# Kernel tuning notes

Measured on AMD Instinct MI355X. Metric: run time of the kernel, lower is better.

Reference implementation:

```python
import jax, jax.numpy as jnp
import numpy as np

SCORE_THR = 0.01
IOU_THR = 0.1          # NOTE: original layer hardcodes 0.1 in tf.image.non_max_suppression
MAX_DET = 100
NEG = jnp.float32(-1e30)


def _iou_one_vs_all(box, boxes):
    # box: [4] (y1,x1,y2,x2), boxes: [N,4]
    y1 = jnp.maximum(box[0], boxes[:, 0])
    x1 = jnp.maximum(box[1], boxes[:, 1])
    y2 = jnp.minimum(box[2], boxes[:, 2])
    x2 = jnp.minimum(box[3], boxes[:, 3])
    inter = jnp.maximum(y2 - y1, 0.0) * jnp.maximum(x2 - x1, 0.0)
    a = (box[2] - box[0]) * (box[3] - box[1])
    b = (boxes[:, 2] - boxes[:, 0]) * (boxes[:, 3] - boxes[:, 1])
    return inter / (a + b - inter + 1e-8)


def _nms_keep(boxes, scores):
    # Greedy NMS as a keep-mask over N anchors. Matches tf.image.non_max_suppression
    # restricted to anchors with score > SCORE_THR, up to MAX_DET selections.
    s = jnp.where(scores > SCORE_THR, scores, NEG)
    keep0 = jnp.zeros(s.shape, dtype=bool)

    def step(carry, _):
        s, keep = carry
        i = jnp.argmax(s)
        ok = s[i] > NEG * 0.5
        keep = keep.at[i].set(ok)
        iou = _iou_one_vs_all(boxes[i], boxes)
        s = jnp.where((iou > IOU_THR) & ok, NEG, s)
        s = s.at[i].set(NEG)
        return (s, keep), None

    (_, keep), _ = jax.lax.scan(step, (s, keep0), None, length=MAX_DET)
    return keep


def _filter_image(boxes_i, cls_i):
    # boxes_i: [N,4], cls_i: [N,C]
    C = cls_i.shape[1]
    # class-specific NMS: keep mask per class -> [C, N]
    keep = jax.vmap(lambda s: _nms_keep(boxes_i, s))(cls_i.T)
    keep_flat = keep.T.reshape(-1)          # [N*C], (anchor, class) flat order
    flat = cls_i.reshape(-1)                # [N*C]
    masked = jnp.where(keep_flat, flat, NEG)
    vals, idx = jax.lax.top_k(masked, MAX_DET)
    valid = vals > NEG * 0.5
    anchor = idx // C
    label = idx % C
    scores_out = jnp.where(valid, jnp.take(flat, idx), -1.0)
    boxes_out = jnp.where(valid[:, None], boxes_i[anchor], -1.0)
    labels_out = jnp.where(valid, label, -1).astype(jnp.int32)
    return boxes_out, scores_out, labels_out


def setup_inputs() -> dict:
    key = jax.random.key(0)
    k1, k2, k3 = jax.random.split(key, 3)
    B, N, C = 4, 49104, 90
    yx1 = jax.random.uniform(k1, (B, N, 2), dtype=jnp.float32) * 512.0
    hw = jax.random.uniform(k2, (B, N, 2), dtype=jnp.float32) * 128.0 + 1.0
    boxes = jnp.concatenate([yx1, yx1 + hw], axis=-1)          # [B,N,4] y1x1y2x2
    classification = jax.random.uniform(k3, (B, N, C), dtype=jnp.float32)
    return {"boxes": boxes, "classification": classification}


def reference(boxes, classification):
    return jax.vmap(_filter_image)(boxes, classification)
```

## Files before the change

### kernel.cpp

```cpp
#include <hip/hip_runtime.h>
#include <stdint.h>

typedef unsigned long long u64;

#define B_ 4
#define N_ 49104
#define C_ 90
#define NCLS (B_ * C_)
#define MAXK 100
#define THR 0.01f
#define NB2 2048
#define WIN 512
#define KCAP 4096
#define ACH 128
#define NCH ((N_ + ACH - 1) / ACH)
#define CAPC 32
#define NBIN_M 1280
#define BINBASE 0x3F6E0000u
#define BINSH_M 10

__device__ __forceinline__ float area_of(float y1, float x1, float y2, float x2) {
#pragma clang fp contract(off)
  return (y2 - y1) * (x2 - x1);
}

#define IOU_MID (26843547.0 / 268435456.0)

__device__ __forceinline__ bool iou_gt(float ay1, float ax1, float ay2, float ax2, float aa,
                                       float by1, float bx1, float by2, float bx2, float ba) {
#pragma clang fp contract(off)
  float y1 = fmaxf(ay1, by1);
  float x1 = fmaxf(ax1, bx1);
  float y2 = fminf(ay2, by2);
  float x2 = fminf(ax2, bx2);
  float inter = fmaxf(y2 - y1, 0.0f) * fmaxf(x2 - x1, 0.0f);
  float denom = aa + ba - inter + 1e-8f;
  return (double)inter >= IOU_MID * (double)denom;
}

__device__ __forceinline__ u64 umax64(u64 a, u64 b) { return a > b ? a : b; }

__device__ __forceinline__ u64 shfl_xor_u64(u64 v, int m) {
  int lo = __shfl_xor((int)(unsigned)v, m);
  int hi = __shfl_xor((int)(unsigned)(v >> 32), m);
  return ((u64)(unsigned)hi << 32) | (u64)(unsigned)lo;
}

__device__ __forceinline__ int key2bin_m(u64 k) {
  int d = (int)((unsigned)(k >> 32) - BINBASE);
  int bin = d >> BINSH_M;
  if (d < 0) bin = 0;
  if (bin > NBIN_M - 1) bin = NBIN_M - 1;
  return bin;
}

__global__ __launch_bounds__(256) void select_kernel(const float* __restrict__ cls,
                                                     u64* __restrict__ keybuf,
                                                     unsigned* __restrict__ cnt,
                                                     int capsel, float t0) {
  __shared__ u64 ll[C_ * CAPC];
  __shared__ unsigned lcnt[C_];
  __shared__ unsigned base_s[C_];
  int blk = blockIdx.x;
  int b = blk / NCH, ch = blk - b * NCH;
  int a0 = ch * ACH;
  int aEnd = a0 + ACH; if (aEnd > N_) aEnd = N_;
  int e0 = a0 * C_;
  int nelem = (aEnd - a0) * C_;
  int tid = threadIdx.x;

  for (int i = tid; i < C_; i += 256) lcnt[i] = 0u;
  __syncthreads();

  const float4* src4 = (const float4*)(cls + (size_t)b * N_ * C_ + e0);
  int n4 = nelem >> 2;
  for (int i4 = tid; i4 < n4; i4 += 256) {
    float4 v = src4[i4];
#pragma unroll
    for (int j = 0; j < 4; ++j) {
      float s = (&v.x)[j];
      if (s > t0) {
        int e = e0 + i4 * 4 + j;
        unsigned n = (unsigned)e / (unsigned)C_;
        unsigned c = (unsigned)e - n * (unsigned)C_;
        u64 key = ((u64)__float_as_uint(s) << 32) | (u64)(0xFFFFFFFFu - n);
        unsigned pos = atomicAdd(&lcnt[c], 1u);
        if (pos < CAPC) {
          ll[c * CAPC + pos] = key;
        } else {
          unsigned g = (unsigned)(b * C_) + c;
          unsigned gp = atomicAdd(&cnt[g * 16], 1u);
          if (gp < (unsigned)capsel) keybuf[(size_t)g * capsel + gp] = key;
        }
      }
    }
  }
  __syncthreads();

  if (tid < C_) {
    unsigned cc = lcnt[tid]; if (cc > CAPC) cc = CAPC;
    base_s[tid] = atomicAdd(&cnt[(b * C_ + tid) * 16], cc);
  }
  __syncthreads();

  for (int i = tid; i < C_ * CAPC; i += 256) {
    int c = i >> 5, j = i & 31;
    unsigned cc = lcnt[c]; if (cc > CAPC) cc = CAPC;
    if ((unsigned)j < cc) {
      unsigned pos = base_s[c] + (unsigned)j;
      if (pos < (unsigned)capsel)
        keybuf[(size_t)(b * C_ + c) * capsel + pos] = ll[i];
    }
  }
}

__global__ __launch_bounds__(512) void nms_kernel(const float* __restrict__ boxes,
                                                  const float* __restrict__ cls,
                                                  const u64* __restrict__ keybuf,
                                                  const unsigned* __restrict__ cnt,
                                                  unsigned* __restrict__ done,
                                                  int capsel, float t0,
                                                  u64* __restrict__ keepkeys,
                                                  int* __restrict__ nk_arr,
                                                  float* __restrict__ out) {
  int gcls = blockIdx.x;
  int b = gcls / C_, c = gcls - b * C_;
  __shared__ u64 karr[KCAP];
  __shared__ unsigned hist[NB2];
  __shared__ unsigned sfx[NB2];
  __shared__ float4 kb[MAXK];
  __shared__ float ka[MAXK];
  __shared__ unsigned wsum[8];
  __shared__ int sh_cnt[8];
  __shared__ int sh_last, sh_thr;
  __shared__ unsigned sh_cc;
  int tid = threadIdx.x;
  int lane = tid & 63;
  int wid = tid >> 6;

  for (int i = tid; i < MAXK; i += 512) keepkeys[(size_t)gcls * MAXK + i] = 0ull;
  for (int i = tid; i < NB2; i += 512) hist[i] = 0u;
  __syncthreads();

  unsigned Mraw = cnt[gcls * 16];
  bool overflow = (Mraw > (unsigned)capsel);
  int M = overflow ? 0 : (int)Mraw;

  const u64* src = keybuf + (size_t)gcls * capsel;

  const int PK = KCAP / 512;
  u64 kreg[PK];
#pragma unroll
  for (int q = 0; q < PK; ++q) {
    kreg[q] = 0ull;
    int i = q * 512 + tid;
    if (i < M) {
      kreg[q] = src[i];
      atomicAdd(&hist[(unsigned)(kreg[q] >> 44) & (NB2 - 1)], 1u);
    }
  }
  __syncthreads();

  {
    const int W = NB2 / 512;
    unsigned loc[W];
    unsigned psum = 0;
#pragma unroll
    for (int q = 0; q < W; ++q) {
      psum += hist[NB2 - 1 - (tid * W + q)];
      loc[q] = psum;
    }
    unsigned incl = psum;
#pragma unroll
    for (int s = 1; s < 64; s <<= 1) {
      unsigned v = (unsigned)__shfl_up((int)incl, s);
      if (lane >= s) incl += v;
    }
    if (lane == 63) wsum[wid] = incl;
    __syncthreads();
    unsigned bs = incl - psum;
    for (int w2 = 0; w2 < wid; ++w2) bs += wsum[w2];
#pragma unroll
    for (int q = 0; q < W; ++q)
      sfx[NB2 - 1 - (tid * W + q)] = bs + loc[q];
  }
  __syncthreads();

#pragma unroll
  for (int q = 0; q < PK; ++q) {
    int i = q * 512 + tid;
    if (i < M) {
      u64 k = kreg[q];
      unsigned bin = (unsigned)(k >> 44) & (NB2 - 1);
      unsigned old = atomicSub(&hist[bin], 1u);
      karr[sfx[bin] - old] = k;
    }
  }
  __syncthreads();

  {
    u64 mk2[PK]; int mt[PK];
#pragma unroll
    for (int q = 0; q < PK; ++q) {
      mk2[q] = 0ull; mt[q] = -1;
      int i = q * 512 + tid;
      if (i < M) {
        u64 k = karr[i];
        int bin = (int)((unsigned)(k >> 44) & (NB2 - 1));
        int hi2 = (int)sfx[bin];
        int lo2 = (bin == NB2 - 1) ? 0 : (int)sfx[bin + 1];
        int r = lo2;
        for (int j = lo2; j < hi2; ++j) r += (karr[j] > k);
        mk2[q] = k; mt[q] = r;
      }
    }
    __syncthreads();
#pragma unroll
    for (int q = 0; q < PK; ++q)
      if (mt[q] >= 0) karr[mt[q]] = mk2[q];
  }
  __syncthreads();

  const float4* bx4 = (const float4*)(boxes + (size_t)b * N_ * 4);

  int seen = 0;
  int nwin = (M + WIN - 1) / WIN;
  for (int w = 0; w < nwin && seen < MAXK; ++w) {
    int base = w * WIN;
    int ci = base + tid;
    bool have = ci < M;
    float4 cb = make_float4(0.f, 0.f, 0.f, 0.f);
    float ca = 0.f;
    if (have) {
      u64 k = karr[ci];
      cb = bx4[0xFFFFFFFFu - (unsigned)(k & 0xFFFFFFFFull)];
      ca = area_of(cb.x, cb.y, cb.z, cb.w);
    }
    bool dead = !have;
    for (int j = 0; j < seen; ++j) {
      float4 sb = kb[j]; float sa = ka[j];
      dead |= iou_gt(sb.x, sb.y, sb.z, sb.w, sa,
                     cb.x, cb.y, cb.z, cb.w, ca);
    }
    u64 alive = __ballot(!dead);

    int nslice = (((M - base) < WIN ? (M - base) : WIN) + 63) >> 6;
    for (int s = 0; s < nslice; ++s) {
      if (wid == s) {
        int nkl = seen;
        int slo = base + (s << 6);
        while (alive != 0ull && nkl < MAXK) {
          int bit = __ffsll((long long)alive) - 1;
          float sy1 = __shfl(cb.x, bit);
          float sx1 = __shfl(cb.y, bit);
          float sy2 = __shfl(cb.z, bit);
          float sx2 = __shfl(cb.w, bit);
          float sa  = __shfl(ca,   bit);
          if (lane == 0) {
            u64 key = karr[slo + bit];
            unsigned anchor = 0xFFFFFFFFu - (unsigned)(key & 0xFFFFFFFFull);
            unsigned flat = anchor * C_ + (unsigned)c;
            keepkeys[(size_t)gcls * MAXK + nkl] =
                (key & 0xFFFFFFFF00000000ull) | (u64)(0xFFFFFFFFu - flat);
            kb[nkl] = make_float4(sy1, sx1, sy2, sx2);
            ka[nkl] = sa;
          }
          ++nkl;
          alive &= ~__ballot(iou_gt(sy1, sx1, sy2, sx2, sa,
                                    cb.x, cb.y, cb.z, cb.w, ca));
        }
        if (lane == 0) sh_cnt[s] = nkl;
        seen = nkl;
      }
      __syncthreads();
      int nkNew = (wid == s) ? seen : sh_cnt[s];
      if (nkNew >= MAXK) { seen = nkNew; break; }
      if (wid > s && nkNew > seen) {
        bool d2 = false;
        for (int j = seen; j < nkNew; ++j) {
          float4 sb = kb[j]; float sa = ka[j];
          d2 |= iou_gt(sb.x, sb.y, sb.z, sb.w, sa,
                       cb.x, cb.y, cb.z, cb.w, ca);
        }
        alive &= __ballot(!d2);
      }
      seen = nkNew;
    }
  }

  int nkF = seen;
  if (nkF < MAXK) {
    float teff = overflow ? 2.0f : t0;
    const float* sbase = cls + (size_t)b * N_ * C_ + c;
    const float* bx = boxes + (size_t)b * N_ * 4;
    u64* kkp = keepkeys + (size_t)gcls * MAXK;
    u64* red = karr;
    int nk2 = nkF;
    while (nk2 < MAXK) {
      u64 best = 0ull;
      for (int n = tid; n < N_; n += 512) {
        float s = sbase[(size_t)n * C_];
        if (s > THR && s <= teff) {
          float y1 = bx[(size_t)n * 4 + 0], x1 = bx[(size_t)n * 4 + 1];
          float y2 = bx[(size_t)n * 4 + 2], x2 = bx[(size_t)n * 4 + 3];
          float ar = area_of(y1, x1, y2, x2);
          bool ov = false;
          for (int j = 0; j < nk2; ++j) {
            float4 kbj = kb[j];
            if (iou_gt(kbj.x, kbj.y, kbj.z, kbj.w, ka[j], y1, x1, y2, x2, ar)) { ov = true; break; }
          }
          if (!ov) {
            u64 key = ((u64)__float_as_uint(s) << 32) | (u64)(0xFFFFFFFFu - (unsigned)n);
            best = umax64(best, key);
          }
        }
      }
      red[tid] = best;
      __syncthreads();
      for (int sft = 256; sft > 0; sft >>= 1) {
        if (tid < sft) red[tid] = umax64(red[tid], red[tid + sft]);
        __syncthreads();
      }
      u64 sel = red[0];
      __syncthreads();
      if (sel == 0ull) {
        if (tid == 0) {
          unsigned target2 = 0xFFFFFFFFu - (unsigned)c;
          for (int j = 0; j < nk2; ++j)
            if ((unsigned)(kkp[j] & 0xFFFFFFFFull) == target2) kkp[j] = 0ull;
        }
        break;
      }
      unsigned anchor = 0xFFFFFFFFu - (unsigned)(sel & 0xFFFFFFFFull);
      if (tid == 0) {
        float y1 = bx[(size_t)anchor * 4 + 0], x1 = bx[(size_t)anchor * 4 + 1];
        float y2 = bx[(size_t)anchor * 4 + 2], x2 = bx[(size_t)anchor * 4 + 3];
        kb[nk2] = make_float4(y1, x1, y2, x2);
        ka[nk2] = area_of(y1, x1, y2, x2);
        unsigned flat = anchor * C_ + (unsigned)c;
        kkp[nk2] = (sel & 0xFFFFFFFF00000000ull) | (u64)(0xFFFFFFFFu - flat);
      }
      ++nk2;
      __syncthreads();
    }
    nkF = nk2;
  }
  if (tid == 0) nk_arr[gcls] = nkF;

  __syncthreads();
  if (tid == 0) {
    __threadfence();
    sh_last = (atomicAdd(&done[b], 1u) == (unsigned)(C_ - 1)) ? 1 : 0;
  }
  __syncthreads();
  if (!sh_last) return;
  __threadfence();

  {
    const u64* kk = keepkeys + (size_t)b * C_ * MAXK;
    const int TOT = C_ * MAXK;
    unsigned* histm = hist;
    unsigned* sfxm = sfx;
    u64* mk = karr;
    u64* selk = karr + 512;

    for (int i = tid; i < NBIN_M; i += 512) histm[i] = 0u;
    if (tid == 0) { sh_thr = -1; sh_cc = 0u; }
    __syncthreads();
    for (int i = tid; i < TOT; i += 512) {
      u64 k = kk[i];
      if (k != 0ull) atomicAdd(&histm[key2bin_m(k)], 1u);
    }
    __syncthreads();

    const int Wm = 3;
    int j0 = tid * Wm;
    unsigned psum = 0;
#pragma unroll
    for (int q = 0; q < Wm; ++q) {
      int bin = NBIN_M - 1 - (j0 + q);
      if (bin >= 0) psum += histm[bin];
    }
    unsigned incl = psum;
#pragma unroll
    for (int s = 1; s < 64; s <<= 1) {
      unsigned v = (unsigned)__shfl_up((int)incl, s);
      if (lane >= s) incl += v;
    }
    if (lane == 63) wsum[wid] = incl;
    __syncthreads();
    unsigned base = incl - psum;
    for (int w2 = 0; w2 < wid; ++w2) base += wsum[w2];
    unsigned running = base;
    int mythr = -1;
#pragma unroll
    for (int q = 0; q < Wm; ++q) {
      int bin = NBIN_M - 1 - (j0 + q);
      if (bin >= 0) {
        running += histm[bin];
        sfxm[bin] = running;
        if (mythr < 0 && running >= (unsigned)MAXK) mythr = bin;
      }
    }
    if (mythr >= 0) atomicMax(&sh_thr, mythr);
    __syncthreads();

    int thr = sh_thr; if (thr < 0) thr = 0;
    unsigned S = sfxm[thr];

    if (S <= 512u) {
      for (int i = tid; i < TOT; i += 512) {
        u64 k = kk[i];
        if (k != 0ull && key2bin_m(k) >= thr) {
          unsigned pos = atomicAdd(&sh_cc, 1u);
          mk[pos] = k;
        }
      }
      __syncthreads();
      for (int i = (int)S + tid; i < 512; i += 512) mk[i] = 0ull;
      __syncthreads();
      for (int k2 = 2; k2 <= 512; k2 <<= 1) {
        for (int j = k2 >> 1; j > 0; j >>= 1) {
          if (tid < 256) {
            int i1 = 2 * tid - (tid & (j - 1));
            int i2 = i1 | j;
            u64 a = mk[i1], bb2 = mk[i2];
            bool desc = ((i1 & k2) == 0);
            bool sw = desc ? (a < bb2) : (a > bb2);
            if (sw) { mk[i1] = bb2; mk[i2] = a; }
          }
          __syncthreads();
        }
      }
      for (int r = tid; r < MAXK; r += 512) selk[r] = mk[r];
      __syncthreads();
    } else {
      if (wid == 0) {
        int c0 = lane, c1 = lane + 64;
        int len0 = (c0 < C_) ? nk_arr[b * C_ + c0] : 0;
        int len1 = (c1 < C_) ? nk_arr[b * C_ + c1] : 0;
        int h0 = 0, h1 = 0;
        auto fetchc = [&](int cc, int& h, int len) -> u64 {
          while (h < len) {
            u64 k = kk[(size_t)cc * MAXK + h];
            if (k != 0ull) return k;
            ++h;
          }
          return 0ull;
        };
        u64 cand0 = (c0 < C_) ? fetchc(c0, h0, len0) : 0ull;
        u64 cand1 = (c1 < C_) ? fetchc(c1, h1, len1) : 0ull;
        for (int r = 0; r < MAXK; ++r) {
          u64 my = umax64(cand0, cand1);
          u64 g = my;
#pragma unroll
          for (int m = 1; m < 64; m <<= 1) g = umax64(g, shfl_xor_u64(g, m));
          if (lane == 0) selk[r] = g;
          if (g != 0ull && my == g) {
            if (cand0 == g) { ++h0; cand0 = fetchc(c0, h0, len0); }
            else            { ++h1; cand1 = fetchc(c1, h1, len1); }
          }
        }
      }
      __syncthreads();
    }

    for (int r = tid; r < MAXK; r += 512) {
      u64 s = selk[r];
      float oy1, ox1, oy2, ox2, sc, lb;
      if (s != 0ull) {
        unsigned flat = 0xFFFFFFFFu - (unsigned)(s & 0xFFFFFFFFull);
        unsigned anchor = flat / C_;
        unsigned label = flat - anchor * C_;
        sc = __uint_as_float((unsigned)(s >> 32));
        const float4 bp = ((const float4*)(boxes + (size_t)b * N_ * 4))[anchor];
        oy1 = bp.x; ox1 = bp.y; oy2 = bp.z; ox2 = bp.w;
        lb = (float)label;
      } else {
        oy1 = ox1 = oy2 = ox2 = -1.0f; sc = -1.0f; lb = -1.0f;
      }
      float* bo = out + ((size_t)b * MAXK + r) * 4;
      bo[0] = oy1; bo[1] = ox1; bo[2] = oy2; bo[3] = ox2;
      out[(size_t)B_ * MAXK * 4 + b * MAXK + r] = sc;
      out[(size_t)B_ * MAXK * 4 + B_ * MAXK + b * MAXK + r] = lb;
    }
  }
}

extern "C" void kernel_launch(void* const* d_in, const int* in_sizes, int n_in,
                              void* d_out, int out_size, void* d_ws, size_t ws_size,
                              hipStream_t stream) {
  const float* boxes = (const float*)d_in[0];
  const float* cls = (const float*)d_in[1];
  char* ws = (char*)d_ws;

  int capsel; float t0;
  auto need_for = [](int cap) -> size_t {
    return 23104 + (size_t)NCLS * cap * 8 + 288000 + 1440;
  };
  if (ws_size >= need_for(4096))      { capsel = 4096; t0 = 0.93f;  }
  else if (ws_size >= need_for(2048)) { capsel = 2048; t0 = 0.962f; }
  else                                { capsel = 1024; t0 = 0.985f; }

  unsigned* cnt = (unsigned*)ws;
  unsigned* done = (unsigned*)(ws + 23040);
  u64* keybuf = (u64*)(ws + 23104);
  size_t off = 23104 + (size_t)NCLS * capsel * 8;
  u64* keepkeys = (u64*)(ws + off);      off += 288000;
  int* nk_arr = (int*)(ws + off);

  hipMemsetAsync(ws, 0, 23104, stream);
  select_kernel<<<B_ * NCH, 256, 0, stream>>>(cls, keybuf, cnt, capsel, t0);
  nms_kernel<<<NCLS, 512, 0, stream>>>(boxes, cls, keybuf, cnt, done, capsel, t0,
                                       keepkeys, nk_arr, (float*)d_out);
}
```

Baseline: 185.5 us.

## Sort and NMS only a top-score prefix per class, fall back to rescan

```diff
diff --git a/kernel.cpp b/kernel.cpp
--- a/kernel.cpp
+++ b/kernel.cpp
@@ -10,8 +10,9 @@
 #define MAXK 100
 #define THR 0.01f
 #define NB2 2048
-#define WIN 512
-#define KCAP 4096
+#define KCAP 640
+#define PTGT 448
+#define PCAP 512
 #define ACH 128
 #define NCH ((N_ + ACH - 1) / ACH)
 #define CAPC 32
@@ -132,6 +133,7 @@
   __shared__ float ka[MAXK];
   __shared__ unsigned wsum[8];
   __shared__ int sh_cnt[8];
+  __shared__ int sh_b1, sh_pl;
   __shared__ int sh_last, sh_thr;
   __shared__ unsigned sh_cc;
   int tid = threadIdx.x;
@@ -140,6 +142,7 @@
 
   for (int i = tid; i < MAXK; i += 512) keepkeys[(size_t)gcls * MAXK + i] = 0ull;
   for (int i = tid; i < NB2; i += 512) hist[i] = 0u;
+  if (tid == 0) sh_b1 = -1;
   __syncthreads();
 
   unsigned Mraw = cnt[gcls * 16];
@@ -148,7 +151,7 @@
 
   const u64* src = keybuf + (size_t)gcls * capsel;
 
-  const int PK = KCAP / 512;
+  const int PK = 4096 / 512;
   u64 kreg[PK];
 #pragma unroll
   for (int q = 0; q < PK; ++q) {
@@ -186,69 +189,83 @@
   }
   __syncthreads();
 
+  if (M > 0) {
+    int target = M < PTGT ? M : PTGT;
+    const int W = NB2 / 512;
+    int mymax = -1;
+#pragma unroll
+    for (int q = 0; q < W; ++q) {
+      int bb = tid * W + q;
+      if ((int)sfx[bb] >= target) mymax = bb > mymax ? bb : mymax;
+    }
+    if (mymax >= 0) atomicMax(&sh_b1, mymax);
+  }
+  __syncthreads();
+  if (tid == 0) {
+    int b1 = sh_b1;
+    int pl = 0;
+    if (M > 0) {
+      pl = (int)sfx[b1];
+      if (pl > PCAP) {
+        ++b1;
+        pl = (b1 < NB2) ? (int)sfx[b1] : 0;
+      }
+    }
+    sh_b1 = b1; sh_pl = pl;
+  }
+  __syncthreads();
+  int b1 = sh_b1;
+  int prefix = sh_pl;
+
 #pragma unroll
   for (int q = 0; q < PK; ++q) {
     int i = q * 512 + tid;
     if (i < M) {
       u64 k = kreg[q];
-      unsigned bin = (unsigned)(k >> 44) & (NB2 - 1);
-      unsigned old = atomicSub(&hist[bin], 1u);
-      karr[sfx[bin] - old] = k;
+      int bin = (int)((unsigned)(k >> 44) & (NB2 - 1));
+      if (bin >= b1) {
+        unsigned old = atomicSub(&hist[bin], 1u);
+        karr[sfx[bin] - old] = k;
+      }
     }
   }
   __syncthreads();
 
   {
-    u64 mk2[PK]; int mt[PK];
-#pragma unroll
-    for (int q = 0; q < PK; ++q) {
-      mk2[q] = 0ull; mt[q] = -1;
-      int i = q * 512 + tid;
-      if (i < M) {
-        u64 k = karr[i];
-        int bin = (int)((unsigned)(k >> 44) & (NB2 - 1));
-        int hi2 = (int)sfx[bin];
-        int lo2 = (bin == NB2 - 1) ? 0 : (int)sfx[bin + 1];
-        int r = lo2;
-        for (int j = lo2; j < hi2; ++j) r += (karr[j] > k);
-        mk2[q] = k; mt[q] = r;
-      }
+    u64 mk2 = 0ull; int mt = -1;
+    if (tid < prefix) {
+      u64 k = karr[tid];
+      int bin = (int)((unsigned)(k >> 44) & (NB2 - 1));
+      int hi2 = (int)sfx[bin];
+      int lo2 = (bin == NB2 - 1) ? 0 : (int)sfx[bin + 1];
+      int r = lo2;
+      for (int j = lo2; j < hi2; ++j) r += (karr[j] > k);
+      mk2 = k; mt = r;
     }
     __syncthreads();
-#pragma unroll
-    for (int q = 0; q < PK; ++q)
-      if (mt[q] >= 0) karr[mt[q]] = mk2[q];
+    if (mt >= 0) karr[mt] = mk2;
   }
   __syncthreads();
 
   const float4* bx4 = (const float4*)(boxes + (size_t)b * N_ * 4);
 
   int seen = 0;
-  int nwin = (M + WIN - 1) / WIN;
-  for (int w = 0; w < nwin && seen < MAXK; ++w) {
-    int base = w * WIN;
-    int ci = base + tid;
-    bool have = ci < M;
+  if (prefix > 0) {
+    bool have = tid < prefix;
     float4 cb = make_float4(0.f, 0.f, 0.f, 0.f);
     float ca = 0.f;
     if (have) {
-      u64 k = karr[ci];
+      u64 k = karr[tid];
       cb = bx4[0xFFFFFFFFu - (unsigned)(k & 0xFFFFFFFFull)];
       ca = area_of(cb.x, cb.y, cb.z, cb.w);
     }
-    bool dead = !have;
-    for (int j = 0; j < seen; ++j) {
-      float4 sb = kb[j]; float sa = ka[j];
-      dead |= iou_gt(sb.x, sb.y, sb.z, sb.w, sa,
-                     cb.x, cb.y, cb.z, cb.w, ca);
-    }
-    u64 alive = __ballot(!dead);
-
-    int nslice = (((M - base) < WIN ? (M - base) : WIN) + 63) >> 6;
+    u64 alive = __ballot(have);
+
+    int nslice = (prefix + 63) >> 6;
     for (int s = 0; s < nslice; ++s) {
       if (wid == s) {
         int nkl = seen;
-        int slo = base + (s << 6);
+        int slo = s << 6;
         while (alive != 0ull && nkl < MAXK) {
           int bit = __ffsll((long long)alive) - 1;
           float sy1 = __shfl(cb.x, bit);
@@ -290,7 +307,11 @@
 
   int nkF = seen;
   if (nkF < MAXK) {
-    float teff = overflow ? 2.0f : t0;
+    float teff;
+    if (overflow)           teff = 2.0f;
+    else if (prefix == 0)   teff = 2.0f;
+    else if (prefix < M)    teff = __uint_as_float(0x3F000000u | (((unsigned)b1 << 12) - 1u));
+    else                    teff = t0;
     const float* sbase = cls + (size_t)b * N_ * C_ + c;
     const float* bx = boxes + (size_t)b * N_ * 4;
     u64* kkp = keepkeys + (size_t)gcls * MAXK;
@@ -365,6 +386,7 @@
     u64* selk = karr + 512;
 
     for (int i = tid; i < NBIN_M; i += 512) histm[i] = 0u;
+    for (int r = tid; r < MAXK; r += 512) selk[r] = 0ull;
     if (tid == 0) { sh_thr = -1; sh_cc = 0u; }
     __syncthreads();
     for (int i = tid; i < TOT; i += 512) {
@@ -417,22 +439,11 @@
         }
       }
       __syncthreads();
-      for (int i = (int)S + tid; i < 512; i += 512) mk[i] = 0ull;
-      __syncthreads();
-      for (int k2 = 2; k2 <= 512; k2 <<= 1) {
-        for (int j = k2 >> 1; j > 0; j >>= 1) {
-          if (tid < 256) {
-            int i1 = 2 * tid - (tid & (j - 1));
-            int i2 = i1 | j;
-            u64 a = mk[i1], bb2 = mk[i2];
-            bool desc = ((i1 & k2) == 0);
-            bool sw = desc ? (a < bb2) : (a > bb2);
-            if (sw) { mk[i1] = bb2; mk[i2] = a; }
-          }
-          __syncthreads();
-        }
-      }
-      for (int r = tid; r < MAXK; r += 512) selk[r] = mk[r];
+      u64 myk = (tid < (int)S) ? mk[tid] : 0ull;
+      int r = 0;
+      for (int j = 0; j < (int)S; ++j) r += (mk[j] > myk);
+      __syncthreads();
+      if (tid < (int)S && r < MAXK) selk[r] = myk;
       __syncthreads();
     } else {
       if (wid == 0) {
@@ -450,12 +461,12 @@
         };
         u64 cand0 = (c0 < C_) ? fetchc(c0, h0, len0) : 0ull;
         u64 cand1 = (c1 < C_) ? fetchc(c1, h1, len1) : 0ull;
-        for (int r = 0; r < MAXK; ++r) {
+        for (int r2 = 0; r2 < MAXK; ++r2) {
           u64 my = umax64(cand0, cand1);
           u64 g = my;
 #pragma unroll
           for (int m = 1; m < 64; m <<= 1) g = umax64(g, shfl_xor_u64(g, m));
-          if (lane == 0) selk[r] = g;
+          if (lane == 0) selk[r2] = g;
           if (g != 0ull && my == g) {
             if (cand0 == g) { ++h0; cand0 = fetchc(c0, h0, len0); }
             else            { ++h1; cand1 = fetchc(c1, h1, len1); }
@@ -465,8 +476,8 @@
       __syncthreads();
     }
 
-    for (int r = tid; r < MAXK; r += 512) {
-      u64 s = selk[r];
+    for (int r2 = tid; r2 < MAXK; r2 += 512) {
+      u64 s = selk[r2];
       float oy1, ox1, oy2, ox2, sc, lb;
       if (s != 0ull) {
         unsigned flat = 0xFFFFFFFFu - (unsigned)(s & 0xFFFFFFFFull);
@@ -479,10 +490,10 @@
       } else {
         oy1 = ox1 = oy2 = ox2 = -1.0f; sc = -1.0f; lb = -1.0f;
       }
-      float* bo = out + ((size_t)b * MAXK + r) * 4;
+      float* bo = out + ((size_t)b * MAXK + r2) * 4;
       bo[0] = oy1; bo[1] = ox1; bo[2] = oy2; bo[3] = ox2;
-      out[(size_t)B_ * MAXK * 4 + b * MAXK + r] = sc;
-      out[(size_t)B_ * MAXK * 4 + B_ * MAXK + b * MAXK + r] = lb;
+      out[(size_t)B_ * MAXK * 4 + b * MAXK + r2] = sc;
+      out[(size_t)B_ * MAXK * 4 + B_ * MAXK + b * MAXK + r2] = lb;
     }
   }
 }
```

New measurement: 176.0 us. 1.05x faster.
